# Kernel tuning notes

Hardware: AMD Instinct MI355X
Metric: run time of the kernel (lower is better)

Reference implementation:

```python
import jax, jax.numpy as jnp
import numpy as np

D_MODEL = 1024
D_STATE = 16
D_CONV = 4
EXPAND = 2
D_INNER = EXPAND * D_MODEL
DT_RANK = (D_MODEL + 15) // 16  # 64
EPS = 1e-5


def dwconv(x, w, b, pad):
    # x: (B, C, L), w: (C, 1, K), depthwise conv
    y = jax.lax.conv_general_dilated(x, w, (1,), [pad],
                                     dimension_numbers=('NCH', 'OIH', 'NCH'),
                                     feature_group_count=x.shape[1])
    return y + b[None, :, None]


def mamba(x, W_inproj, m_conv_w, m_conv_b, W_xproj, W_dt, b_dt, A_log, Dp, W_outproj):
    # x: (B, L, d_model)
    Bn, L, _ = x.shape
    xz = x @ W_inproj.T                       # (B, L, 2*d_inner)
    xi, z = jnp.split(xz, 2, axis=-1)
    # causal depthwise conv: pad (K-1, 0) == torch pad K-1 then slice [:L]
    xc = dwconv(jnp.swapaxes(xi, 1, 2), m_conv_w, m_conv_b, (D_CONV - 1, 0))
    u = jax.nn.silu(jnp.swapaxes(xc, 1, 2))   # (B, L, d_inner)
    x_dbl = u @ W_xproj.T                     # (B, L, dt_rank + 2*d_state)
    dt = x_dbl[..., :DT_RANK]
    Bm = x_dbl[..., DT_RANK:DT_RANK + D_STATE]
    Cm = x_dbl[..., DT_RANK + D_STATE:]
    dt = jax.nn.softplus(dt @ W_dt.T + b_dt)  # (B, L, d_inner)
    A = -jnp.exp(A_log)                       # (d_inner, d_state)

    def step(h, inp):
        dt_t, B_t, C_t, u_t = inp             # (B,di),(B,ds),(B,ds),(B,di)
        dA = jnp.exp(dt_t[..., None] * A)     # (B, di, ds)
        h = dA * h + dt_t[..., None] * B_t[:, None, :] * u_t[..., None]
        y = jnp.einsum('bds,bs->bd', h, C_t)
        return h, y

    tm = lambda a: jnp.swapaxes(a, 0, 1)      # time-major for scan
    h0 = jnp.zeros((Bn, D_INNER, D_STATE), x.dtype)
    _, ys = jax.lax.scan(step, h0, (tm(dt), tm(Bm), tm(Cm), tm(u)))
    y = jnp.swapaxes(ys, 0, 1) + u * Dp       # (B, L, d_inner)
    y = y * jax.nn.silu(z)
    return y @ W_outproj.T                    # (B, L, d_model)


def forward(x, ln_g, ln_b, W_in, b_in, conv_w, conv_b,
            W_inproj, m_conv_w, m_conv_b, W_xproj, W_dt, b_dt,
            A_log, Dp, W_outproj, W_out, b_out):
    h = jnp.swapaxes(x, 1, 2)                 # (B, L, d_model)
    mu = h.mean(-1, keepdims=True)
    var = ((h - mu) ** 2).mean(-1, keepdims=True)
    h = (h - mu) / jnp.sqrt(var + EPS) * ln_g + ln_b
    h = h @ W_in.T + b_in
    # outer depthwise conv: kernel 4, pad 2 each side -> length L+1 (faithful)
    h = dwconv(jnp.swapaxes(h, 1, 2), conv_w, conv_b, (D_CONV // 2, D_CONV // 2))
    h = jax.nn.silu(h)
    h = jnp.swapaxes(h, 1, 2)                 # (B, L+1, d_model)
    y = mamba(h, W_inproj, m_conv_w, m_conv_b, W_xproj, W_dt, b_dt, A_log, Dp, W_outproj)
    y = y @ W_out.T + b_out
    return jnp.swapaxes(y, 1, 2)              # (B, d_model, L+1)


def setup_inputs() -> dict:
    key = jax.random.key(0)
    ks = jax.random.split(key, 16)
    B, L = 2, 2048
    s = 0.02
    inp = {
        'x': jax.random.normal(ks[0], (B, D_MODEL, L), jnp.float32),
        'ln_g': jnp.ones((D_MODEL,), jnp.float32),
        'ln_b': jnp.zeros((D_MODEL,), jnp.float32),
        'W_in': jax.random.normal(ks[1], (D_MODEL, D_MODEL), jnp.float32) * s,
        'b_in': jnp.zeros((D_MODEL,), jnp.float32),
        'conv_w': jax.random.normal(ks[2], (D_MODEL, 1, D_CONV), jnp.float32) * 0.3,
        'conv_b': jnp.zeros((D_MODEL,), jnp.float32),
        'W_inproj': jax.random.normal(ks[3], (2 * D_INNER, D_MODEL), jnp.float32) * s,
        'm_conv_w': jax.random.normal(ks[4], (D_INNER, 1, D_CONV), jnp.float32) * 0.3,
        'm_conv_b': jnp.zeros((D_INNER,), jnp.float32),
        'W_xproj': jax.random.normal(ks[5], (DT_RANK + 2 * D_STATE, D_INNER), jnp.float32) * s,
        'W_dt': jax.random.normal(ks[6], (D_INNER, DT_RANK), jnp.float32) * (DT_RANK ** -0.5),
        'b_dt': jax.random.uniform(ks[7], (D_INNER,), jnp.float32, -4.6, -2.0),
        'A_log': jnp.log(jnp.tile(jnp.arange(1, D_STATE + 1, dtype=jnp.float32)[None, :], (D_INNER, 1))),
        'Dp': jnp.ones((D_INNER,), jnp.float32),
        'W_outproj': jax.random.normal(ks[8], (D_MODEL, D_INNER), jnp.float32) * s,
        'W_out': jax.random.normal(ks[9], (D_MODEL, D_MODEL), jnp.float32) * s,
        'b_out': jnp.zeros((D_MODEL,), jnp.float32),
    }
    return inp


def reference(x, ln_g, ln_b, W_in, b_in, conv_w, conv_b, W_inproj, m_conv_w, m_conv_b,
              W_xproj, W_dt, b_dt, A_log, Dp, W_outproj, W_out, b_out):
    return forward(x, ln_g, ln_b, W_in, b_in, conv_w, conv_b, W_inproj, m_conv_w,
                   m_conv_b, W_xproj, W_dt, b_dt, A_log, Dp, W_outproj, W_out, b_out)
```

## Files before the change

kernel.cpp:

```cpp
#include <hip/hip_runtime.h>
#include <hip/hip_bf16.h>

#define DMODEL 1024
#define DINNER 2048
#define DTRANK 64
#define NPROJ  96
#define BATCH  2
#define LIN    2048
#define LOUT   2049
#define MTOT0  4096
#define MTOT1  4098
#define TC     64
#define NCH    33

typedef __attribute__((ext_vector_type(8))) short short8;
typedef __attribute__((ext_vector_type(4))) float f32x4;

__device__ __forceinline__ float f_silu(float x)     { return x / (1.f + __expf(-x)); }
__device__ __forceinline__ float f_softplus(float x) { return (x > 20.f) ? x : log1pf(__expf(x)); }
__device__ __forceinline__ short f2b(float x)
{
    __hip_bfloat16 b = __float2bfloat16(x);
    return *reinterpret_cast<short*>(&b);
}

__global__ void ln_stats_k(const float* __restrict__ x, float* __restrict__ mu, float* __restrict__ rs)
{
    int b  = blockIdx.y;
    int l0 = blockIdx.x * 64;
    int lc = threadIdx.x & 63;
    int q  = threadIdx.x >> 6;
    const float* xb = x + (size_t)b * DMODEL * LIN + (l0 + lc);
    float s = 0.f, ss = 0.f;
    for (int c = q * 256; c < q * 256 + 256; ++c) {
        float v = xb[(size_t)c * LIN];
        s += v; ss += v * v;
    }
    __shared__ float Ss[4][64];
    __shared__ float Sq[4][64];
    Ss[q][lc] = s; Sq[q][lc] = ss;
    __syncthreads();
    if (threadIdx.x < 64) {
        float st = Ss[0][lc] + Ss[1][lc] + Ss[2][lc] + Ss[3][lc];
        float sq = Sq[0][lc] + Sq[1][lc] + Sq[2][lc] + Sq[3][lc];
        float m = st * (1.f / DMODEL);
        float v = sq * (1.f / DMODEL) - m * m;
        mu[b * LIN + l0 + lc] = m;
        rs[b * LIN + l0 + lc] = 1.f / sqrtf(v + 1e-5f);
    }
}

__global__ void lnT_k(const float* __restrict__ x, const float* __restrict__ mu,
                      const float* __restrict__ rs, const float* __restrict__ g,
                      const float* __restrict__ be, short* __restrict__ h0T)
{
    __shared__ float T[32][33];
    int l0 = blockIdx.x * 32;
    int c0 = blockIdx.y * 32;
    int b  = blockIdx.z;
    int tx = threadIdx.x & 31, ty = threadIdx.x >> 5;
    const float* xb = x + ((size_t)b * DMODEL + c0) * LIN + l0;
#pragma unroll
    for (int i = 0; i < 4; i++) {
        int cl = ty + 8 * i;
        T[cl][tx] = xb[(size_t)cl * LIN + tx];
    }
    __syncthreads();
    int c = c0 + tx;
    float gg = g[c], bb = be[c];
#pragma unroll
    for (int i = 0; i < 4; i++) {
        int ll = ty + 8 * i;
        int m = b * LIN + l0 + ll;
        float v = (T[tx][ll] - mu[m]) * rs[m] * gg + bb;
        h0T[(size_t)m * DMODEL + c] = f2b(v);
    }
}

__global__ void cvt_k(const float* __restrict__ src, short* __restrict__ dst, int n)
{
    int i = (blockIdx.x * 256 + threadIdx.x) * 4;
    if (i + 3 < n) {
        float4 v = *(const float4*)(src + i);
        dst[i + 0] = f2b(v.x); dst[i + 1] = f2b(v.y);
        dst[i + 2] = f2b(v.z); dst[i + 3] = f2b(v.w);
    } else {
        for (int e = 0; e < 4 && i + e < n; e++) dst[i + e] = f2b(src[i + e]);
    }
}

template<int EPI>
__global__ __launch_bounds__(256) void gemm_bf(
    const short* __restrict__ A, int lda,
    const short* __restrict__ W, int ldb,
    float* __restrict__ C, int ldc,
    short* __restrict__ Cb, int ldcb,
    int M, int N, int K,
    const float* __restrict__ bias)
{
    __shared__ short As[128][40];
    __shared__ short Bs[128][40];
    int tid  = threadIdx.x;
    int lane = tid & 63, wid = tid >> 6;
    int wr = wid >> 1, wc = wid & 1;
    int fr = lane & 15, kg = lane >> 4;
    int m0 = blockIdx.x * 128, n0 = blockIdx.y * 128;
    int sr = tid >> 1, sh = (tid & 1) * 16;

    f32x4 acc[4][4];
#pragma unroll
    for (int mi = 0; mi < 4; mi++)
#pragma unroll
        for (int ni = 0; ni < 4; ni++) acc[mi][ni] = (f32x4){0.f, 0.f, 0.f, 0.f};

    const short8 zz = {0, 0, 0, 0, 0, 0, 0, 0};

    for (int k0 = 0; k0 < K; k0 += 32) {
        short8 a0 = zz, a1 = zz, b0 = zz, b1 = zz;
        if (m0 + sr < M) {
            const short* p = A + (size_t)(m0 + sr) * lda + k0 + sh;
            a0 = *(const short8*)p;
            a1 = *(const short8*)(p + 8);
        }
        if (n0 + sr < N) {
            const short* p = W + (size_t)(n0 + sr) * ldb + k0 + sh;
            b0 = *(const short8*)p;
            b1 = *(const short8*)(p + 8);
        }
        *(short8*)&As[sr][sh]     = a0;
        *(short8*)&As[sr][sh + 8] = a1;
        *(short8*)&Bs[sr][sh]     = b0;
        *(short8*)&Bs[sr][sh + 8] = b1;
        __syncthreads();

        short8 af[4], bfr[4];
#pragma unroll
        for (int mi = 0; mi < 4; mi++)
            af[mi] = *(const short8*)&As[wr * 64 + mi * 16 + fr][kg * 8];
#pragma unroll
        for (int ni = 0; ni < 4; ni++)
            bfr[ni] = *(const short8*)&Bs[wc * 64 + ni * 16 + fr][kg * 8];
#pragma unroll
        for (int mi = 0; mi < 4; mi++)
#pragma unroll
            for (int ni = 0; ni < 4; ni++)
                acc[mi][ni] = __builtin_amdgcn_mfma_f32_16x16x32_bf16(
                    af[mi], bfr[ni], acc[mi][ni], 0, 0, 0);
        __syncthreads();
    }

#pragma unroll
    for (int ni = 0; ni < 4; ni++) {
        int n = n0 + wc * 64 + ni * 16 + fr;
        if (n >= N) continue;
        float bv = 0.f;
        if (EPI == 1 || EPI == 2) bv = bias[n];
#pragma unroll
        for (int mi = 0; mi < 4; mi++) {
#pragma unroll
            for (int r = 0; r < 4; r++) {
                int m = m0 + wr * 64 + mi * 16 + kg * 4 + r;
                if (m >= M) continue;
                float v = acc[mi][ni][r];
                if (EPI == 1) v += bv;
                if (EPI == 2) v = f_softplus(v + bv);
                if (EPI == 5) {
                    float vb = v + bias[m];
                    int bq = (n >= LOUT) ? 1 : 0;
                    int l  = n - bq * LOUT;
                    C[((size_t)bq * DMODEL + m) * LOUT + l] = vb;
                } else if (EPI == 4) {
                    Cb[(size_t)m * ldcb + n] = f2b(v);
                } else {
                    C[(size_t)m * ldc + n] = v;
                    if (EPI == 3 && n < DTRANK) Cb[(size_t)m * ldcb + n] = f2b(v);
                }
            }
        }
    }
}

__global__ void conv1_k(const float* __restrict__ h1, const float* __restrict__ cw,
                        const float* __restrict__ cb, short* __restrict__ h2b)
{
    int c = blockIdx.x * 256 + threadIdx.x;
    int m = blockIdx.y;
    int b = (m >= LOUT) ? 1 : 0;
    int l = m - b * LOUT;
    float4 wv = ((const float4*)cw)[c];
    const float* w = (const float*)&wv;
    float acc = cb[c];
#pragma unroll
    for (int k = 0; k < 4; k++) {
        int li = l - 2 + k;
        if (li >= 0 && li < LIN)
            acc += h1[((size_t)b * LIN + li) * DMODEL + c] * w[k];
    }
    h2b[(size_t)m * DMODEL + c] = f2b(f_silu(acc));
}

__global__ void conv2_k(const float* __restrict__ xz, const float* __restrict__ cw,
                        const float* __restrict__ cb, float* __restrict__ u,
                        short* __restrict__ ub)
{
    int d = blockIdx.x * 256 + threadIdx.x;
    int m = blockIdx.y;
    int b = (m >= LOUT) ? 1 : 0;
    int l = m - b * LOUT;
    float4 wv = ((const float4*)cw)[d];
    const float* w = (const float*)&wv;
    float acc = cb[d];
#pragma unroll
    for (int k = 0; k < 4; k++) {
        int li = l - 3 + k;
        if (li >= 0)
            acc += xz[((size_t)b * LOUT + li) * (2 * DINNER) + d] * w[k];
    }
    float s = f_silu(acc);
    u [(size_t)m * DINNER + d] = s;
    ub[(size_t)m * DINNER + d] = f2b(s);
}

__global__ void scan1_k(const float* __restrict__ dt, const float* __restrict__ u,
                        const float* __restrict__ xdbl, const float* __restrict__ A_log,
                        float* __restrict__ sP, float* __restrict__ sH)
{
    int d = blockIdx.x * 256 + threadIdx.x;
    int c = blockIdx.y;
    int b = blockIdx.z;
    int t0 = c * TC;
    int tlen = LOUT - t0; if (tlen > TC) tlen = TC;

    float Ad[16], h[16], P[16];
#pragma unroll
    for (int q = 0; q < 4; q++) {
        float4 av = ((const float4*)A_log)[d * 4 + q];
        Ad[q*4+0] = -__expf(av.x); Ad[q*4+1] = -__expf(av.y);
        Ad[q*4+2] = -__expf(av.z); Ad[q*4+3] = -__expf(av.w);
    }
#pragma unroll
    for (int s = 0; s < 16; s++) { h[s] = 0.f; P[s] = 1.f; }

    size_t row0 = (size_t)b * LOUT + t0;
    const float* dtp = dt + row0 * DINNER + d;
    const float* up  = u  + row0 * DINNER + d;
    const float* Bp  = xdbl + row0 * NPROJ + DTRANK;
    for (int t = 0; t < tlen; t++) {
        float dtt = dtp[(size_t)t * DINNER];
        float du  = dtt * up[(size_t)t * DINNER];
        const float* Bt = Bp + (size_t)t * NPROJ;
#pragma unroll
        for (int s = 0; s < 16; s++) {
            float a = __expf(dtt * Ad[s]);
            h[s] = a * h[s] + du * Bt[s];
            P[s] *= a;
        }
    }
    size_t base = ((size_t)(b * NCH + c) * 16) * DINNER + d;
#pragma unroll
    for (int s = 0; s < 16; s++) {
        sP[base + (size_t)s * DINNER] = P[s];
        sH[base + (size_t)s * DINNER] = h[s];
    }
}

__global__ void scan2_k(const float* __restrict__ sP, float* __restrict__ sH)
{
    int gid = blockIdx.x * 256 + threadIdx.x;
    int d = gid & (DINNER - 1);
    int s = (gid >> 11) & 15;
    int b = gid >> 15;
    size_t base = ((size_t)(b * NCH) * 16 + s) * DINNER + d;
    const size_t cstep = (size_t)16 * DINNER;
    float hrun = 0.f;
    for (int c = 0; c < NCH; c++) {
        size_t idx = base + (size_t)c * cstep;
        float Pv = sP[idx], hl = sH[idx];
        sH[idx] = hrun;
        hrun = Pv * hrun + hl;
    }
}

__global__ void scan3_k(const float* __restrict__ dt, const float* __restrict__ u,
                        const float* __restrict__ xdbl, const float* __restrict__ A_log,
                        const float* __restrict__ Dp, const float* __restrict__ xz,
                        const float* __restrict__ sH, short* __restrict__ ymb)
{
    int d = blockIdx.x * 256 + threadIdx.x;
    int c = blockIdx.y;
    int b = blockIdx.z;
    int t0 = c * TC;
    int tlen = LOUT - t0; if (tlen > TC) tlen = TC;

    float Ad[16], h[16];
#pragma unroll
    for (int q = 0; q < 4; q++) {
        float4 av = ((const float4*)A_log)[d * 4 + q];
        Ad[q*4+0] = -__expf(av.x); Ad[q*4+1] = -__expf(av.y);
        Ad[q*4+2] = -__expf(av.z); Ad[q*4+3] = -__expf(av.w);
    }
    size_t sbase = ((size_t)(b * NCH + c) * 16) * DINNER + d;
#pragma unroll
    for (int s = 0; s < 16; s++) h[s] = sH[sbase + (size_t)s * DINNER];

    float Dpd = Dp[d];
    size_t row0 = (size_t)b * LOUT + t0;
    const float* dtp = dt + row0 * DINNER + d;
    const float* up  = u  + row0 * DINNER + d;
    const float* Bp  = xdbl + row0 * NPROJ + DTRANK;
    const float* Cp  = Bp + 16;
    const float* zp  = xz + row0 * (2 * DINNER) + DINNER + d;
    short* yp = ymb + row0 * DINNER + d;
    for (int t = 0; t < tlen; t++) {
        float dtt = dtp[(size_t)t * DINNER];
        float ut  = up[(size_t)t * DINNER];
        float du  = dtt * ut;
        const float* Bt = Bp + (size_t)t * NPROJ;
        const float* Ct = Cp + (size_t)t * NPROJ;
        float y = 0.f;
#pragma unroll
        for (int s = 0; s < 16; s++) {
            float a = __expf(dtt * Ad[s]);
            h[s] = a * h[s] + du * Bt[s];
            y += h[s] * Ct[s];
        }
        float z = zp[(size_t)t * (2 * DINNER)];
        yp[(size_t)t * DINNER] = f2b((y + ut * Dpd) * f_silu(z));
    }
}

extern "C" void kernel_launch(void* const* d_in, const int* in_sizes, int n_in,
                              void* d_out, int out_size, void* d_ws, size_t ws_size,
                              hipStream_t stream)
{
    (void)in_sizes; (void)n_in; (void)out_size; (void)ws_size;
    const float* x        = (const float*)d_in[0];
    const float* ln_g     = (const float*)d_in[1];
    const float* ln_b     = (const float*)d_in[2];
    const float* W_in     = (const float*)d_in[3];
    const float* b_in     = (const float*)d_in[4];
    const float* conv_w   = (const float*)d_in[5];
    const float* conv_b   = (const float*)d_in[6];
    const float* W_inproj = (const float*)d_in[7];
    const float* m_conv_w = (const float*)d_in[8];
    const float* m_conv_b = (const float*)d_in[9];
    const float* W_xproj  = (const float*)d_in[10];
    const float* W_dt     = (const float*)d_in[11];
    const float* b_dt     = (const float*)d_in[12];
    const float* A_log    = (const float*)d_in[13];
    const float* Dp       = (const float*)d_in[14];
    const float* W_outproj= (const float*)d_in[15];
    const float* W_out    = (const float*)d_in[16];
    const float* b_out    = (const float*)d_in[17];
    float* out = (float*)d_out;

    float* F    = (float*)d_ws;
    float* mu   = F;
    float* rs   = F + 4096;
    float* h1   = F + 8192;
    float* xz   = h1 + (size_t)MTOT0 * DMODEL;
    float* uu   = xz + (size_t)MTOT1 * 2 * DINNER;
    float* xdbl = uu + (size_t)MTOT1 * DINNER;
    float* dt   = xdbl + (size_t)MTOT1 * NPROJ;
    float* sP   = dt + (size_t)MTOT1 * DINNER;
    float* sH   = sP + (size_t)BATCH * NCH * 16 * DINNER;
    float* fend = sH + (size_t)BATCH * NCH * 16 * DINNER;

    short* S     = (short*)fend;
    short* h0T   = S;
    short* h2b   = h0T + (size_t)MTOT0 * DMODEL;
    short* ub    = h2b + (size_t)MTOT1 * DMODEL;
    short* Wib   = ub  + (size_t)MTOT1 * DINNER;
    short* Winpb = Wib   + (size_t)DMODEL * DMODEL;
    short* Wxpb  = Winpb + (size_t)(2*DINNER) * DMODEL;
    short* Wdtb  = Wxpb  + (size_t)NPROJ * DINNER;
    short* Wopb  = Wdtb  + (size_t)DINNER * DTRANK;
    short* Wob   = Wopb  + (size_t)DMODEL * DINNER;
    short* dtin  = h0T;
    short* ymb   = ub;
    short* o1b   = (short*)h1;

    cvt_k<<<1024, 256, 0, stream>>>(W_in,      Wib,   DMODEL * DMODEL);
    cvt_k<<<4096, 256, 0, stream>>>(W_inproj,  Winpb, 2 * DINNER * DMODEL);
    cvt_k<<<192,  256, 0, stream>>>(W_xproj,   Wxpb,  NPROJ * DINNER);
    cvt_k<<<128,  256, 0, stream>>>(W_dt,      Wdtb,  DINNER * DTRANK);
    cvt_k<<<2048, 256, 0, stream>>>(W_outproj, Wopb,  DMODEL * DINNER);
    cvt_k<<<1024, 256, 0, stream>>>(W_out,     Wob,   DMODEL * DMODEL);
    ln_stats_k<<<dim3(32, 2), 256, 0, stream>>>(x, mu, rs);
    lnT_k<<<dim3(64, 32, 2), 256, 0, stream>>>(x, mu, rs, ln_g, ln_b, h0T);
    gemm_bf<1><<<dim3(32, 8), 256, 0, stream>>>(h0T, DMODEL, Wib, DMODEL,
        h1, DMODEL, nullptr, 0, MTOT0, DMODEL, DMODEL, b_in);
    conv1_k<<<dim3(4, MTOT1), 256, 0, stream>>>(h1, conv_w, conv_b, h2b);
    gemm_bf<0><<<dim3(33, 32), 256, 0, stream>>>(h2b, DMODEL, Winpb, DMODEL,
        xz, 2 * DINNER, nullptr, 0, MTOT1, 2 * DINNER, DMODEL, nullptr);
    conv2_k<<<dim3(8, MTOT1), 256, 0, stream>>>(xz, m_conv_w, m_conv_b, uu, ub);
    gemm_bf<3><<<dim3(33, 1), 256, 0, stream>>>(ub, DINNER, Wxpb, DINNER,
        xdbl, NPROJ, dtin, DTRANK, MTOT1, NPROJ, DINNER, nullptr);
    gemm_bf<2><<<dim3(33, 16), 256, 0, stream>>>(dtin, DTRANK, Wdtb, DTRANK,
        dt, DINNER, nullptr, 0, MTOT1, DINNER, DTRANK, b_dt);
    scan1_k<<<dim3(8, NCH, 2), 256, 0, stream>>>(dt, uu, xdbl, A_log, sP, sH);
    scan2_k<<<dim3(256), 256, 0, stream>>>(sP, sH);
    scan3_k<<<dim3(8, NCH, 2), 256, 0, stream>>>(dt, uu, xdbl, A_log, Dp, xz, sH, ymb);
    gemm_bf<4><<<dim3(33, 8), 256, 0, stream>>>(ymb, DINNER, Wopb, DINNER,
        nullptr, 0, o1b, DMODEL, MTOT1, DMODEL, DINNER, nullptr);
    gemm_bf<5><<<dim3(8, 33), 256, 0, stream>>>(Wob, DMODEL, o1b, DMODEL,
        out, 0, nullptr, 0, DMODEL, MTOT1, DMODEL, b_out);
}
```

Baseline: 675.1 us.

## Load GEMM tiles directly into LDS, fuse dt projection, merge weight conversions

The bf16 GEMM now stages A/B tiles with global_load_lds 16-byte direct-to-LDS loads instead of going through registers. The LDS tiles drop their padding, and the M/N bounds checks on loads are removed. The six weight-conversion launches are merged into one kernel. The dt low-rank projection plus softplus becomes a dedicated fp32 kernel reading xdbl directly, replacing the bf16 copy and a separate GEMM. The aim is less register staging and fewer launches, at the risk of LDS bank conflicts from the unpadded layout and of out-of-range tile reads past M and N.

New measurement: 603.4 us. -10.6%, faster.

```diff
diff --git a/kernel.cpp b/kernel.cpp
--- a/kernel.cpp
+++ b/kernel.cpp
@@ -23,6 +23,17 @@
     __hip_bfloat16 b = __float2bfloat16(x);
     return *reinterpret_cast<short*>(&b);
 }
+__device__ __forceinline__ float b2f(short s)
+{
+    return __uint_as_float(((unsigned)(unsigned short)s) << 16);
+}
+__device__ __forceinline__ void gload16(const void* g, void* l)
+{
+    __builtin_amdgcn_global_load_lds(
+        (const __attribute__((address_space(1))) void*)g,
+        (__attribute__((address_space(3))) void*)l,
+        16, 0, 0);
+}
 
 __global__ void ln_stats_k(const float* __restrict__ x, float* __restrict__ mu, float* __restrict__ rs)
 {
@@ -77,16 +88,25 @@
     }
 }
 
-__global__ void cvt_k(const float* __restrict__ src, short* __restrict__ dst, int n)
-{
-    int i = (blockIdx.x * 256 + threadIdx.x) * 4;
-    if (i + 3 < n) {
-        float4 v = *(const float4*)(src + i);
-        dst[i + 0] = f2b(v.x); dst[i + 1] = f2b(v.y);
-        dst[i + 2] = f2b(v.z); dst[i + 3] = f2b(v.w);
-    } else {
-        for (int e = 0; e < 4 && i + e < n; e++) dst[i + e] = f2b(src[i + e]);
-    }
+__global__ void cvt_all_k(const float* __restrict__ W_in, const float* __restrict__ W_inproj,
+                          const float* __restrict__ W_xproj, const float* __restrict__ W_dt,
+                          const float* __restrict__ W_outproj, const float* __restrict__ W_out,
+                          short* __restrict__ Wib, short* __restrict__ Winpb,
+                          short* __restrict__ Wxpb, short* __restrict__ Wdtb,
+                          short* __restrict__ Wopb, short* __restrict__ Wob)
+{
+    int b = blockIdx.x;
+    const float* s; short* d; int i;
+    if      (b < 1024) { s = W_in;      d = Wib;   i = b; }
+    else if (b < 5120) { s = W_inproj;  d = Winpb; i = b - 1024; }
+    else if (b < 5312) { s = W_xproj;   d = Wxpb;  i = b - 5120; }
+    else if (b < 5440) { s = W_dt;      d = Wdtb;  i = b - 5312; }
+    else if (b < 7488) { s = W_outproj; d = Wopb;  i = b - 5440; }
+    else               { s = W_out;     d = Wob;   i = b - 7488; }
+    int idx = (i * 256 + threadIdx.x) * 4;
+    float4 v = *(const float4*)(s + idx);
+    d[idx + 0] = f2b(v.x); d[idx + 1] = f2b(v.y);
+    d[idx + 2] = f2b(v.z); d[idx + 3] = f2b(v.w);
 }
 
 template<int EPI>
@@ -98,14 +118,25 @@
     int M, int N, int K,
     const float* __restrict__ bias)
 {
-    __shared__ short As[128][40];
-    __shared__ short Bs[128][40];
+    __shared__ short As[128 * 32];
+    __shared__ short Bs[128 * 32];
     int tid  = threadIdx.x;
     int lane = tid & 63, wid = tid >> 6;
     int wr = wid >> 1, wc = wid & 1;
     int fr = lane & 15, kg = lane >> 4;
     int m0 = blockIdx.x * 128, n0 = blockIdx.y * 128;
-    int sr = tid >> 1, sh = (tid & 1) * 16;
+
+    int scol  = (lane & 3) * 8;
+    int srow0 = wid * 32 + (lane >> 2);
+    int srow1 = srow0 + 16;
+    const short* a0 = A + (size_t)(m0 + srow0) * lda + scol;
+    const short* a1 = A + (size_t)(m0 + srow1) * lda + scol;
+    const short* b0 = W + (size_t)(n0 + srow0) * ldb + scol;
+    const short* b1 = W + (size_t)(n0 + srow1) * ldb + scol;
+    char* asd0 = (char*)As + (wid * 2 + 0) * 1024;
+    char* asd1 = (char*)As + (wid * 2 + 1) * 1024;
+    char* bsd0 = (char*)Bs + (wid * 2 + 0) * 1024;
+    char* bsd1 = (char*)Bs + (wid * 2 + 1) * 1024;
 
     f32x4 acc[4][4];
 #pragma unroll
@@ -113,39 +144,26 @@
 #pragma unroll
         for (int ni = 0; ni < 4; ni++) acc[mi][ni] = (f32x4){0.f, 0.f, 0.f, 0.f};
 
-    const short8 zz = {0, 0, 0, 0, 0, 0, 0, 0};
-
     for (int k0 = 0; k0 < K; k0 += 32) {
-        short8 a0 = zz, a1 = zz, b0 = zz, b1 = zz;
-        if (m0 + sr < M) {
-            const short* p = A + (size_t)(m0 + sr) * lda + k0 + sh;
-            a0 = *(const short8*)p;
-            a1 = *(const short8*)(p + 8);
-        }
-        if (n0 + sr < N) {
-            const short* p = W + (size_t)(n0 + sr) * ldb + k0 + sh;
-            b0 = *(const short8*)p;
-            b1 = *(const short8*)(p + 8);
-        }
-        *(short8*)&As[sr][sh]     = a0;
-        *(short8*)&As[sr][sh + 8] = a1;
-        *(short8*)&Bs[sr][sh]     = b0;
-        *(short8*)&Bs[sr][sh + 8] = b1;
+        gload16(a0 + k0, asd0);
+        gload16(a1 + k0, asd1);
+        gload16(b0 + k0, bsd0);
+        gload16(b1 + k0, bsd1);
         __syncthreads();
 
-        short8 af[4], bfr[4];
+        short8 af[4], bf[4];
 #pragma unroll
         for (int mi = 0; mi < 4; mi++)
-            af[mi] = *(const short8*)&As[wr * 64 + mi * 16 + fr][kg * 8];
+            af[mi] = *(const short8*)&As[(wr * 64 + mi * 16 + fr) * 32 + kg * 8];
 #pragma unroll
         for (int ni = 0; ni < 4; ni++)
-            bfr[ni] = *(const short8*)&Bs[wc * 64 + ni * 16 + fr][kg * 8];
+            bf[ni] = *(const short8*)&Bs[(wc * 64 + ni * 16 + fr) * 32 + kg * 8];
 #pragma unroll
         for (int mi = 0; mi < 4; mi++)
 #pragma unroll
             for (int ni = 0; ni < 4; ni++)
                 acc[mi][ni] = __builtin_amdgcn_mfma_f32_16x16x32_bf16(
-                    af[mi], bfr[ni], acc[mi][ni], 0, 0, 0);
+                    af[mi], bf[ni], acc[mi][ni], 0, 0, 0);
         __syncthreads();
     }
 
@@ -154,7 +172,7 @@
         int n = n0 + wc * 64 + ni * 16 + fr;
         if (n >= N) continue;
         float bv = 0.f;
-        if (EPI == 1 || EPI == 2) bv = bias[n];
+        if (EPI == 1) bv = bias[n];
 #pragma unroll
         for (int mi = 0; mi < 4; mi++) {
 #pragma unroll
@@ -163,7 +181,6 @@
                 if (m >= M) continue;
                 float v = acc[mi][ni][r];
                 if (EPI == 1) v += bv;
-                if (EPI == 2) v = f_softplus(v + bv);
                 if (EPI == 5) {
                     float vb = v + bias[m];
                     int bq = (n >= LOUT) ? 1 : 0;
@@ -173,10 +190,62 @@
                     Cb[(size_t)m * ldcb + n] = f2b(v);
                 } else {
                     C[(size_t)m * ldc + n] = v;
-                    if (EPI == 3 && n < DTRANK) Cb[(size_t)m * ldcb + n] = f2b(v);
                 }
             }
         }
+    }
+}
+
+__global__ __launch_bounds__(256) void dtfuse_k(const float* __restrict__ xdbl,
+                                                const short* __restrict__ Wdtb,
+                                                const float* __restrict__ b_dt,
+                                                float* __restrict__ dtout)
+{
+    int t  = threadIdx.x;
+    int m0 = blockIdx.x * 4;
+    __shared__ float dr[4][64];
+    int mr = m0 + (t >> 6);
+    dr[t >> 6][t & 63] = (mr < MTOT1) ? xdbl[(size_t)mr * NPROJ + (t & 63)] : 0.f;
+    __syncthreads();
+
+    int n = t * 8;
+    float acc[4][8];
+#pragma unroll
+    for (int j = 0; j < 8; j++) {
+        float bj = b_dt[n + j];
+#pragma unroll
+        for (int mi = 0; mi < 4; mi++) acc[mi][j] = bj;
+    }
+    for (int kk = 0; kk < 64; kk += 8) {
+        float w[8][8];
+#pragma unroll
+        for (int j = 0; j < 8; j++) {
+            short8 wv = *(const short8*)&Wdtb[(size_t)(n + j) * 64 + kk];
+#pragma unroll
+            for (int e = 0; e < 8; e++) w[j][e] = b2f(wv[e]);
+        }
+#pragma unroll
+        for (int mi = 0; mi < 4; mi++) {
+            float d[8];
+#pragma unroll
+            for (int e = 0; e < 8; e++) d[e] = dr[mi][kk + e];
+#pragma unroll
+            for (int j = 0; j < 8; j++)
+#pragma unroll
+                for (int e = 0; e < 8; e++) acc[mi][j] += d[e] * w[j][e];
+        }
+    }
+#pragma unroll
+    for (int mi = 0; mi < 4; mi++) {
+        int m = m0 + mi;
+        if (m >= MTOT1) continue;
+        float4 o0, o1;
+        o0.x = f_softplus(acc[mi][0]); o0.y = f_softplus(acc[mi][1]);
+        o0.z = f_softplus(acc[mi][2]); o0.w = f_softplus(acc[mi][3]);
+        o1.x = f_softplus(acc[mi][4]); o1.y = f_softplus(acc[mi][5]);
+        o1.z = f_softplus(acc[mi][6]); o1.w = f_softplus(acc[mi][7]);
+        *(float4*)&dtout[(size_t)m * DINNER + n]     = o0;
+        *(float4*)&dtout[(size_t)m * DINNER + n + 4] = o1;
     }
 }
 
@@ -376,16 +445,11 @@
     short* Wdtb  = Wxpb  + (size_t)NPROJ * DINNER;
     short* Wopb  = Wdtb  + (size_t)DINNER * DTRANK;
     short* Wob   = Wopb  + (size_t)DMODEL * DINNER;
-    short* dtin  = h0T;
     short* ymb   = ub;
     short* o1b   = (short*)h1;
 
-    cvt_k<<<1024, 256, 0, stream>>>(W_in,      Wib,   DMODEL * DMODEL);
-    cvt_k<<<4096, 256, 0, stream>>>(W_inproj,  Winpb, 2 * DINNER * DMODEL);
-    cvt_k<<<192,  256, 0, stream>>>(W_xproj,   Wxpb,  NPROJ * DINNER);
-    cvt_k<<<128,  256, 0, stream>>>(W_dt,      Wdtb,  DINNER * DTRANK);
-    cvt_k<<<2048, 256, 0, stream>>>(W_outproj, Wopb,  DMODEL * DINNER);
-    cvt_k<<<1024, 256, 0, stream>>>(W_out,     Wob,   DMODEL * DMODEL);
+    cvt_all_k<<<8512, 256, 0, stream>>>(W_in, W_inproj, W_xproj, W_dt, W_outproj, W_out,
+                                        Wib, Winpb, Wxpb, Wdtb, Wopb, Wob);
     ln_stats_k<<<dim3(32, 2), 256, 0, stream>>>(x, mu, rs);
     lnT_k<<<dim3(64, 32, 2), 256, 0, stream>>>(x, mu, rs, ln_g, ln_b, h0T);
     gemm_bf<1><<<dim3(32, 8), 256, 0, stream>>>(h0T, DMODEL, Wib, DMODEL,
@@ -394,10 +458,9 @@
     gemm_bf<0><<<dim3(33, 32), 256, 0, stream>>>(h2b, DMODEL, Winpb, DMODEL,
         xz, 2 * DINNER, nullptr, 0, MTOT1, 2 * DINNER, DMODEL, nullptr);
     conv2_k<<<dim3(8, MTOT1), 256, 0, stream>>>(xz, m_conv_w, m_conv_b, uu, ub);
-    gemm_bf<3><<<dim3(33, 1), 256, 0, stream>>>(ub, DINNER, Wxpb, DINNER,
-        xdbl, NPROJ, dtin, DTRANK, MTOT1, NPROJ, DINNER, nullptr);
-    gemm_bf<2><<<dim3(33, 16), 256, 0, stream>>>(dtin, DTRANK, Wdtb, DTRANK,
-        dt, DINNER, nullptr, 0, MTOT1, DINNER, DTRANK, b_dt);
+    gemm_bf<0><<<dim3(33, 1), 256, 0, stream>>>(ub, DINNER, Wxpb, DINNER,
+        xdbl, NPROJ, nullptr, 0, MTOT1, NPROJ, DINNER, nullptr);
+    dtfuse_k<<<1025, 256, 0, stream>>>(xdbl, Wdtb, b_dt, dt);
     scan1_k<<<dim3(8, NCH, 2), 256, 0, stream>>>(dt, uu, xdbl, A_log, sP, sH);
     scan2_k<<<dim3(256), 256, 0, stream>>>(sP, sH);
     scan3_k<<<dim3(8, NCH, 2), 256, 0, stream>>>(dt, uu, xdbl, A_log, Dp, xz, sH, ymb);
```
